# Kernel tuning notes

Measured on AMD Instinct MI355X. Metric: run time of the kernel, lower is better.

## Reference

```python
import jax, jax.numpy as jnp
import numpy as np


def setup_inputs() -> dict:
    key = jax.random.key(0)
    k1, k2, k3, k4, k5 = jax.random.split(key, 5)
    B, C, H, W = 8, 32, 64, 64
    inp = jax.random.normal(k1, (B, C, H, W), dtype=jnp.float32)
    # expected positions lie inside the image grid
    exPx = jax.random.uniform(k2, (B, H, W), dtype=jnp.float32) * (W - 1)
    exPy = jax.random.uniform(k3, (B, H, W), dtype=jnp.float32) * (H - 1)
    # positive Gaussian widths in roughly [1, 3]
    sigmax = jax.random.uniform(k4, (B, H, W), dtype=jnp.float32) * 2.0 + 1.0
    sigmay = jax.random.uniform(k5, (B, H, W), dtype=jnp.float32) * 2.0 + 1.0
    return {"input": inp, "exPx": exPx, "exPy": exPy,
            "sigmax": sigmax, "sigmay": sigmay}


def reference(input, exPx, exPy, sigmax, sigmay):
    """Gaussian-weighted spatial swap/warp (soft gather).

    For each output pixel (i, j):
      out[b,c,i,j] = sum_{u,v} G(u; exPy[b,i,j], sigmay[b,i,j])
                              * G(v; exPx[b,i,j], sigmax[b,i,j])
                              * input[b,c,u,v]  /  Z[b,i,j]
    where G is an unnormalized Gaussian and Z is the total weight mass.
    The 2D Gaussian weight is separable, so we contract rows then cols.
    """
    B, C, H, W = input.shape
    u = jnp.arange(H, dtype=input.dtype)  # source row coords (y)
    v = jnp.arange(W, dtype=input.dtype)  # source col coords (x)
    # wy: [B,H,W,H] weight over source rows u for each output pixel (i,j)
    wy = jnp.exp(-0.5 * ((u[None, None, None, :] - exPy[..., None]) / sigmay[..., None]) ** 2)
    # wx: [B,H,W,W] weight over source cols v
    wx = jnp.exp(-0.5 * ((v[None, None, None, :] - exPx[..., None]) / sigmax[..., None]) ** 2)
    # normalization mass per output pixel
    Z = wy.sum(-1) * wx.sum(-1) + jnp.asarray(1e-8, input.dtype)  # [B,H,W]
    # contract over source rows u -> [B,C,H,W,W]
    t = jnp.einsum('biju,bcuv->bcijv', wy, input)
    # contract over source cols v -> [B,C,H,W]
    out = jnp.einsum('bcijv,bijv->bcij', t, wx)
    return out / Z[:, None]
```

## Files before the change

### kernel.cpp

```cpp
#include <hip/hip_runtime.h>


#define BB 8
#define CC 32
#define HH 64
#define WW 64

typedef __attribute__((ext_vector_type(8))) short short8;
typedef __attribute__((ext_vector_type(4))) float f32x4;
typedef unsigned int uint;

__device__ __forceinline__ uint rn_bf16(float f) {
    uint u = __float_as_uint(f);
    return (u + 0x7FFFu + ((u >> 16) & 1u)) >> 16;
}

__global__ void preconvert_kernel(const float* __restrict__ x, uint* __restrict__ hi)
{
    const int n = BB * CC * HH * WW / 2;
    int idx = blockIdx.x * blockDim.x + threadIdx.x;
    for (; idx < n; idx += gridDim.x * blockDim.x) {
        const float2 d = ((const float2*)x)[idx];
        hi[idx] = rn_bf16(d.x) | (rn_bf16(d.y) << 16);
    }
}

#define WYS_OFF   0
#define WXH_OFF   16640
#define SUM_OFF   25856
#define INVZ_OFF  27904
#define LDS_BYTES 28160
#define RED_OFF   0

__global__ __launch_bounds__(256, 4)
void swap_mfma_kernel(const uint* __restrict__ xhi,
                      const float* __restrict__ exPx, const float* __restrict__ exPy,
                      const float* __restrict__ sigmax, const float* __restrict__ sigmay,
                      float* __restrict__ out)
{
    __shared__ __align__(16) char lds[LDS_BYTES];
    const int t    = threadIdx.x;
    const int lane = t & 63;
    const int w    = t >> 6;
    const int q    = (t >> 4) & 3;
    const int ln   = t & 15;
    const int bid   = blockIdx.x;
    const int b     = bid & 7;
    const int r     = bid >> 3;
    const int chalf = r & 1;
    const int i     = r >> 1;
    const int bi    = b * 64 + i;

    float* WYS = (float*)(lds + WYS_OFF);

    {
        const int p = lane;
        const int g = w;
        const int pixBase = bi * 64 + p;
        const float ey = exPy[pixBase], ex = exPx[pixBase];
        const float isy = 1.0f / sigmay[pixBase], isx = 1.0f / sigmax[pixBase];
        float sy = 0.0f, sx = 0.0f;
        #pragma unroll
        for (int k = 0; k < 16; ++k) {
            const int u = g * 16 + k;
            const float dy = ((float)u - ey) * isy;
            const float wy = __expf(-0.5f * dy * dy);
            WYS[u * 65 + p] = wy;
            sy += wy;
        }
        uint* WXH = (uint*)(lds + WXH_OFF);
        #pragma unroll
        for (int j = 0; j < 8; ++j) {
            const int v0 = g * 16 + 2 * j;
            const float dx0 = ((float)v0       - ex) * isx;
            const float dx1 = ((float)(v0 + 1) - ex) * isx;
            const float wx0 = __expf(-0.5f * dx0 * dx0);
            const float wx1 = __expf(-0.5f * dx1 * dx1);
            sx += wx0 + wx1;
            WXH[p * 36 + g * 8 + j] = rn_bf16(wx0) | (rn_bf16(wx1) << 16);
        }
        float* SUMY = (float*)(lds + SUM_OFF);
        float* SUMX = SUMY + 256;
        SUMY[g * 64 + p] = sy;
        SUMX[g * 64 + p] = sx;
    }
    __syncthreads();
    float* INVZ = (float*)(lds + INVZ_OFF);
    if (t < 64) {
        float* SUMY = (float*)(lds + SUM_OFF);
        float* SUMX = SUMY + 256;
        const float sy = SUMY[t] + SUMY[64 + t] + SUMY[128 + t] + SUMY[192 + t];
        const float sx = SUMX[t] + SUMX[64 + t] + SUMX[128 + t] + SUMX[192 + t];
        INVZ[t] = 1.0f / (sy * sx + 1e-8f);
    }
    __syncthreads();

    short8 bh[4][2];
    #pragma unroll
    for (int nt = 0; nt < 4; ++nt)
        #pragma unroll
        for (int ks = 0; ks < 2; ++ks)
            bh[nt][ks] = *(const short8*)(lds + WXH_OFF + (nt * 16 + ln) * 144 + ks * 64 + q * 16);
    float wyz[4][4];
    #pragma unroll
    for (int nt = 0; nt < 4; ++nt) {
        const float iz = INVZ[nt * 16 + ln];
        #pragma unroll
        for (int rr = 0; rr < 4; ++rr)
            wyz[nt][rr] = WYS[(w * 16 + q * 4 + rr) * 65 + nt * 16 + ln] * iz;
    }
    __syncthreads();

    const int cbase = b * CC + chalf * 16;
    float* RED = (float*)(lds + RED_OFF);
    const uint* xrow = xhi + (size_t)cbase * 2048 + (w * 16 + ln) * 32 + q * 4;

    #pragma unroll 4
    for (int c = 0; c < 16; ++c) {
        const uint4* src = (const uint4*)(xrow + (size_t)c * 2048);
        union { uint4 v; short8 s; } A0, A1;
        A0.v = src[0];
        A1.v = src[4];

        f32x4 acc[4];
        #pragma unroll
        for (int nt = 0; nt < 4; ++nt) acc[nt] = (f32x4){0.f, 0.f, 0.f, 0.f};
        #pragma unroll
        for (int nt = 0; nt < 4; ++nt) {
            acc[nt] = __builtin_amdgcn_mfma_f32_16x16x32_bf16(A0.s, bh[nt][0], acc[nt], 0, 0, 0);
            acc[nt] = __builtin_amdgcn_mfma_f32_16x16x32_bf16(A1.s, bh[nt][1], acc[nt], 0, 0, 0);
        }
        #pragma unroll
        for (int nt = 0; nt < 4; ++nt) {
            float ps = acc[nt][0] * wyz[nt][0] + acc[nt][1] * wyz[nt][1]
                     + acc[nt][2] * wyz[nt][2] + acc[nt][3] * wyz[nt][3];
            ps += __shfl_xor(ps, 16, 64);
            ps += __shfl_xor(ps, 32, 64);
            if (q == 0) RED[c * 256 + w * 64 + nt * 16 + ln] = ps;
        }
    }
    __syncthreads();

    {
        const int kk = t >> 6, p = t & 63;
        #pragma unroll
        for (int g = 0; g < 4; ++g) {
            const int c = g * 4 + kk;
            const float* Rk = RED + c * 256;
            const float o = Rk[p] + Rk[64 + p] + Rk[128 + p] + Rk[192 + p];
            out[(size_t)(cbase + c) * (HH * WW) + i * 64 + p] = o;
        }
    }
}

__device__ __forceinline__ void split_pair(float f0, float f1, uint& hi, uint& lo) {
    const uint u0 = __float_as_uint(f0), u1 = __float_as_uint(f1);
    hi = (u0 >> 16) | (u1 & 0xFFFF0000u);
    const float l0 = f0 - __uint_as_float(u0 & 0xFFFF0000u);
    const float l1 = f1 - __uint_as_float(u1 & 0xFFFF0000u);
    lo = (__float_as_uint(l0) >> 16) | (__float_as_uint(l1) & 0xFFFF0000u);
}

__global__ __launch_bounds__(256, 4)
void swap_fused_kernel(const float* __restrict__ inp,
                       const float* __restrict__ exPx, const float* __restrict__ exPy,
                       const float* __restrict__ sigmax, const float* __restrict__ sigmay,
                       float* __restrict__ out)
{
    __shared__ __align__(16) char lds[LDS_BYTES];
    const int t = threadIdx.x;
    const int lane = t & 63, w = t >> 6, q = (t >> 4) & 3, ln = t & 15;
    const int bid = blockIdx.x;
    const int b = bid & 7, r = bid >> 3;
    const int chalf = r & 1, i = r >> 1;
    const int bi = b * 64 + i;

    float* WYS = (float*)(lds + WYS_OFF);
    {
        const int p = lane, g = w;
        const int pixBase = bi * 64 + p;
        const float ey = exPy[pixBase], ex = exPx[pixBase];
        const float isy = 1.0f / sigmay[pixBase], isx = 1.0f / sigmax[pixBase];
        float sy = 0.0f, sx = 0.0f;
        #pragma unroll
        for (int k = 0; k < 16; ++k) {
            const int u = g * 16 + k;
            const float dy = ((float)u - ey) * isy;
            const float wy = __expf(-0.5f * dy * dy);
            WYS[u * 65 + p] = wy; sy += wy;
        }
        uint* WXH = (uint*)(lds + WXH_OFF);
        #pragma unroll
        for (int j = 0; j < 8; ++j) {
            const int v0 = g * 16 + 2 * j;
            const float dx0 = ((float)v0 - ex) * isx;
            const float dx1 = ((float)(v0 + 1) - ex) * isx;
            const float wx0 = __expf(-0.5f * dx0 * dx0);
            const float wx1 = __expf(-0.5f * dx1 * dx1);
            sx += wx0 + wx1;
            WXH[p * 36 + g * 8 + j] = rn_bf16(wx0) | (rn_bf16(wx1) << 16);
        }
        float* SUMY = (float*)(lds + SUM_OFF);
        float* SUMX = SUMY + 256;
        SUMY[g * 64 + p] = sy; SUMX[g * 64 + p] = sx;
    }
    __syncthreads();
    float* INVZ = (float*)(lds + INVZ_OFF);
    if (t < 64) {
        float* SUMY = (float*)(lds + SUM_OFF);
        float* SUMX = SUMY + 256;
        const float sy = SUMY[t] + SUMY[64 + t] + SUMY[128 + t] + SUMY[192 + t];
        const float sx = SUMX[t] + SUMX[64 + t] + SUMX[128 + t] + SUMX[192 + t];
        INVZ[t] = 1.0f / (sy * sx + 1e-8f);
    }
    __syncthreads();
    short8 bh[4][2];
    #pragma unroll
    for (int nt = 0; nt < 4; ++nt)
        #pragma unroll
        for (int ks = 0; ks < 2; ++ks)
            bh[nt][ks] = *(const short8*)(lds + WXH_OFF + (nt * 16 + ln) * 144 + ks * 64 + q * 16);
    float wyz[4][4];
    #pragma unroll
    for (int nt = 0; nt < 4; ++nt) {
        const float iz = INVZ[nt * 16 + ln];
        #pragma unroll
        for (int rr = 0; rr < 4; ++rr)
            wyz[nt][rr] = WYS[(w * 16 + q * 4 + rr) * 65 + nt * 16 + ln] * iz;
    }
    __syncthreads();
    const int cbase = b * CC + chalf * 16;
    float* RED = (float*)(lds + RED_OFF);
    const float* xrow = inp + (size_t)cbase * 4096 + (w * 16 + ln) * 64 + q * 8;
    #pragma unroll 2
    for (int c = 0; c < 16; ++c) {
        const float4* src = (const float4*)(xrow + (size_t)c * 4096);
        const float4 x0 = src[0], x1 = src[1], x2 = src[8], x3 = src[9];
        union { uint u[4]; short8 s; } Ah0, Al0, Ah1, Al1;
        split_pair(x0.x, x0.y, Ah0.u[0], Al0.u[0]);
        split_pair(x0.z, x0.w, Ah0.u[1], Al0.u[1]);
        split_pair(x1.x, x1.y, Ah0.u[2], Al0.u[2]);
        split_pair(x1.z, x1.w, Ah0.u[3], Al0.u[3]);
        split_pair(x2.x, x2.y, Ah1.u[0], Al1.u[0]);
        split_pair(x2.z, x2.w, Ah1.u[1], Al1.u[1]);
        split_pair(x3.x, x3.y, Ah1.u[2], Al1.u[2]);
        split_pair(x3.z, x3.w, Ah1.u[3], Al1.u[3]);
        f32x4 acc[4];
        #pragma unroll
        for (int nt = 0; nt < 4; ++nt) acc[nt] = (f32x4){0.f, 0.f, 0.f, 0.f};
        #pragma unroll
        for (int nt = 0; nt < 4; ++nt) {
            acc[nt] = __builtin_amdgcn_mfma_f32_16x16x32_bf16(Ah0.s, bh[nt][0], acc[nt], 0, 0, 0);
            acc[nt] = __builtin_amdgcn_mfma_f32_16x16x32_bf16(Al0.s, bh[nt][0], acc[nt], 0, 0, 0);
            acc[nt] = __builtin_amdgcn_mfma_f32_16x16x32_bf16(Ah1.s, bh[nt][1], acc[nt], 0, 0, 0);
            acc[nt] = __builtin_amdgcn_mfma_f32_16x16x32_bf16(Al1.s, bh[nt][1], acc[nt], 0, 0, 0);
        }
        #pragma unroll
        for (int nt = 0; nt < 4; ++nt) {
            float ps = acc[nt][0] * wyz[nt][0] + acc[nt][1] * wyz[nt][1]
                     + acc[nt][2] * wyz[nt][2] + acc[nt][3] * wyz[nt][3];
            ps += __shfl_xor(ps, 16, 64);
            ps += __shfl_xor(ps, 32, 64);
            if (q == 0) RED[c * 256 + w * 64 + nt * 16 + ln] = ps;
        }
    }
    __syncthreads();
    {
        const int kk = t >> 6, p = t & 63;
        #pragma unroll
        for (int g = 0; g < 4; ++g) {
            const int c = g * 4 + kk;
            const float* Rk = RED + c * 256;
            const float o = Rk[p] + Rk[64 + p] + Rk[128 + p] + Rk[192 + p];
            out[(size_t)(cbase + c) * (HH * WW) + i * 64 + p] = o;
        }
    }
}

extern "C" void kernel_launch(void* const* d_in, const int* in_sizes, int n_in,
                              void* d_out, int out_size, void* d_ws, size_t ws_size,
                              hipStream_t stream) {
    const float* inp    = (const float*)d_in[0];
    const float* exPx   = (const float*)d_in[1];
    const float* exPy   = (const float*)d_in[2];
    const float* sigmax = (const float*)d_in[3];
    const float* sigmay = (const float*)d_in[4];
    float* out = (float*)d_out;

    const size_t plane_bytes = (size_t)BB * CC * HH * WW * 2;
    if (ws_size >= plane_bytes) {
        uint* xhi = (uint*)d_ws;
        hipLaunchKernelGGL(preconvert_kernel, dim3(1024), dim3(256), 0, stream, inp, xhi);
        hipLaunchKernelGGL(swap_mfma_kernel, dim3(BB * HH * 2), dim3(256), 0, stream,
                           xhi, exPx, exPy, sigmax, sigmay, out);
    } else {
        hipLaunchKernelGGL(swap_fused_kernel, dim3(BB * HH * 2), dim3(256), 0, stream,
                           inp, exPx, exPy, sigmax, sigmay, out);
    }
}
```

Before: 82.25 us.

## Split channels across waves so each wave owns full rows, drop LDS reduction

The MFMA kernel now assigns four channels per wave, with each wave covering all 64 source rows through four M-tiles, instead of each wave covering 16 rows for all 16 channels. This removes the cross-wave LDS reduction buffer, the final syncthreads and the gather pass, and outputs are written directly after scaling by 1/Z. The Y-weights are stored transposed in LDS with float4 rows and read per tile inside the loop rather than cached in registers. The tradeoffs are more LDS reads in the inner loop, larger A-fragment register pressure, and a channel loop that is no longer unrolled.

Measured after the change: 97.01 us. 17.9% more time.

```diff
diff --git a/kernel.cpp b/kernel.cpp
--- a/kernel.cpp
+++ b/kernel.cpp
@@ -25,12 +25,11 @@
     }
 }
 
-#define WYS_OFF   0
-#define WXH_OFF   16640
-#define SUM_OFF   25856
-#define INVZ_OFF  27904
-#define LDS_BYTES 28160
-#define RED_OFF   0
+#define WYT_OFF   0
+#define WXH_OFF   17408
+#define SUM_OFF   26624
+#define INVZ_OFF  28672
+#define LDS_BYTES 28928
 
 __global__ __launch_bounds__(256, 4)
 void swap_mfma_kernel(const uint* __restrict__ xhi,
@@ -51,7 +50,7 @@
     const int i     = r >> 1;
     const int bi    = b * 64 + i;
 
-    float* WYS = (float*)(lds + WYS_OFF);
+    float* WYT = (float*)(lds + WYT_OFF);
 
     {
         const int p = lane;
@@ -61,12 +60,17 @@
         const float isy = 1.0f / sigmay[pixBase], isx = 1.0f / sigmax[pixBase];
         float sy = 0.0f, sx = 0.0f;
         #pragma unroll
-        for (int k = 0; k < 16; ++k) {
-            const int u = g * 16 + k;
-            const float dy = ((float)u - ey) * isy;
-            const float wy = __expf(-0.5f * dy * dy);
-            WYS[u * 65 + p] = wy;
-            sy += wy;
+        for (int jb = 0; jb < 4; ++jb) {
+            float4 wv;
+            #pragma unroll
+            for (int rr = 0; rr < 4; ++rr) {
+                const int u = g * 16 + jb * 4 + rr;
+                const float dy = ((float)u - ey) * isy;
+                const float wy = __expf(-0.5f * dy * dy);
+                ((float*)&wv)[rr] = wy;
+                sy += wy;
+            }
+            *(float4*)&WYT[p * 68 + g * 16 + jb * 4] = wv;
         }
         uint* WXH = (uint*)(lds + WXH_OFF);
         #pragma unroll
@@ -101,54 +105,37 @@
         #pragma unroll
         for (int ks = 0; ks < 2; ++ks)
             bh[nt][ks] = *(const short8*)(lds + WXH_OFF + (nt * 16 + ln) * 144 + ks * 64 + q * 16);
-    float wyz[4][4];
-    #pragma unroll
-    for (int nt = 0; nt < 4; ++nt) {
-        const float iz = INVZ[nt * 16 + ln];
-        #pragma unroll
-        for (int rr = 0; rr < 4; ++rr)
-            wyz[nt][rr] = WYS[(w * 16 + q * 4 + rr) * 65 + nt * 16 + ln] * iz;
-    }
-    __syncthreads();
-
-    const int cbase = b * CC + chalf * 16;
-    float* RED = (float*)(lds + RED_OFF);
-    const uint* xrow = xhi + (size_t)cbase * 2048 + (w * 16 + ln) * 32 + q * 4;
-
-    #pragma unroll 4
-    for (int c = 0; c < 16; ++c) {
-        const uint4* src = (const uint4*)(xrow + (size_t)c * 2048);
-        union { uint4 v; short8 s; } A0, A1;
-        A0.v = src[0];
-        A1.v = src[4];
-
-        f32x4 acc[4];
-        #pragma unroll
-        for (int nt = 0; nt < 4; ++nt) acc[nt] = (f32x4){0.f, 0.f, 0.f, 0.f};
+    float invz[4];
+    #pragma unroll
+    for (int nt = 0; nt < 4; ++nt) invz[nt] = INVZ[nt * 16 + ln];
+
+    const int cplane0 = b * CC + chalf * 16 + w * 4;
+    const uint* xbase = xhi + (size_t)cplane0 * 2048 + ln * 32 + q * 4;
+    float* obase = out + (size_t)cplane0 * 4096 + i * 64 + ln;
+
+    for (int c = 0; c < 4; ++c) {
+        const uint* xc = xbase + c * 2048;
+        union { uint4 v; short8 s; } A[4][2];
+        #pragma unroll
+        for (int mt = 0; mt < 4; ++mt) {
+            A[mt][0].v = *(const uint4*)(xc + mt * 512);
+            A[mt][1].v = *(const uint4*)(xc + mt * 512 + 16);
+        }
         #pragma unroll
         for (int nt = 0; nt < 4; ++nt) {
-            acc[nt] = __builtin_amdgcn_mfma_f32_16x16x32_bf16(A0.s, bh[nt][0], acc[nt], 0, 0, 0);
-            acc[nt] = __builtin_amdgcn_mfma_f32_16x16x32_bf16(A1.s, bh[nt][1], acc[nt], 0, 0, 0);
-        }
-        #pragma unroll
-        for (int nt = 0; nt < 4; ++nt) {
-            float ps = acc[nt][0] * wyz[nt][0] + acc[nt][1] * wyz[nt][1]
-                     + acc[nt][2] * wyz[nt][2] + acc[nt][3] * wyz[nt][3];
+            float ps = 0.0f;
+            #pragma unroll
+            for (int mt = 0; mt < 4; ++mt) {
+                f32x4 acc = (f32x4){0.f, 0.f, 0.f, 0.f};
+                acc = __builtin_amdgcn_mfma_f32_16x16x32_bf16(A[mt][0].s, bh[nt][0], acc, 0, 0, 0);
+                acc = __builtin_amdgcn_mfma_f32_16x16x32_bf16(A[mt][1].s, bh[nt][1], acc, 0, 0, 0);
+                const f32x4 wv = *(const f32x4*)&WYT[(nt * 16 + ln) * 68 + mt * 16 + q * 4];
+                ps += acc[0] * wv[0] + acc[1] * wv[1] + acc[2] * wv[2] + acc[3] * wv[3];
+            }
             ps += __shfl_xor(ps, 16, 64);
             ps += __shfl_xor(ps, 32, 64);
-            if (q == 0) RED[c * 256 + w * 64 + nt * 16 + ln] = ps;
-        }
-    }
-    __syncthreads();
-
-    {
-        const int kk = t >> 6, p = t & 63;
-        #pragma unroll
-        for (int g = 0; g < 4; ++g) {
-            const int c = g * 4 + kk;
-            const float* Rk = RED + c * 256;
-            const float o = Rk[p] + Rk[64 + p] + Rk[128 + p] + Rk[192 + p];
-            out[(size_t)(cbase + c) * (HH * WW) + i * 64 + p] = o;
+            if (q == 0)
+                obase[(size_t)c * 4096 + nt * 16] = ps * invz[nt];
         }
     }
 }
@@ -161,13 +148,20 @@
     lo = (__float_as_uint(l0) >> 16) | (__float_as_uint(l1) & 0xFFFF0000u);
 }
 
+#define FB_WYS_OFF   0
+#define FB_WXH_OFF   16640
+#define FB_SUM_OFF   25856
+#define FB_INVZ_OFF  27904
+#define FB_LDS_BYTES 28160
+#define FB_RED_OFF   0
+
 __global__ __launch_bounds__(256, 4)
 void swap_fused_kernel(const float* __restrict__ inp,
                        const float* __restrict__ exPx, const float* __restrict__ exPy,
                        const float* __restrict__ sigmax, const float* __restrict__ sigmay,
                        float* __restrict__ out)
 {
-    __shared__ __align__(16) char lds[LDS_BYTES];
+    __shared__ __align__(16) char lds[FB_LDS_BYTES];
     const int t = threadIdx.x;
     const int lane = t & 63, w = t >> 6, q = (t >> 4) & 3, ln = t & 15;
     const int bid = blockIdx.x;
@@ -175,7 +169,7 @@
     const int chalf = r & 1, i = r >> 1;
     const int bi = b * 64 + i;
 
-    float* WYS = (float*)(lds + WYS_OFF);
+    float* WYS = (float*)(lds + FB_WYS_OFF);
     {
         const int p = lane, g = w;
         const int pixBase = bi * 64 + p;
@@ -189,7 +183,7 @@
             const float wy = __expf(-0.5f * dy * dy);
             WYS[u * 65 + p] = wy; sy += wy;
         }
-        uint* WXH = (uint*)(lds + WXH_OFF);
+        uint* WXH = (uint*)(lds + FB_WXH_OFF);
         #pragma unroll
         for (int j = 0; j < 8; ++j) {
             const int v0 = g * 16 + 2 * j;
@@ -200,14 +194,14 @@
             sx += wx0 + wx1;
             WXH[p * 36 + g * 8 + j] = rn_bf16(wx0) | (rn_bf16(wx1) << 16);
         }
-        float* SUMY = (float*)(lds + SUM_OFF);
+        float* SUMY = (float*)(lds + FB_SUM_OFF);
         float* SUMX = SUMY + 256;
         SUMY[g * 64 + p] = sy; SUMX[g * 64 + p] = sx;
     }
     __syncthreads();
-    float* INVZ = (float*)(lds + INVZ_OFF);
+    float* INVZ = (float*)(lds + FB_INVZ_OFF);
     if (t < 64) {
-        float* SUMY = (float*)(lds + SUM_OFF);
+        float* SUMY = (float*)(lds + FB_SUM_OFF);
         float* SUMX = SUMY + 256;
         const float sy = SUMY[t] + SUMY[64 + t] + SUMY[128 + t] + SUMY[192 + t];
         const float sx = SUMX[t] + SUMX[64 + t] + SUMX[128 + t] + SUMX[192 + t];
@@ -219,7 +213,7 @@
     for (int nt = 0; nt < 4; ++nt)
         #pragma unroll
         for (int ks = 0; ks < 2; ++ks)
-            bh[nt][ks] = *(const short8*)(lds + WXH_OFF + (nt * 16 + ln) * 144 + ks * 64 + q * 16);
+            bh[nt][ks] = *(const short8*)(lds + FB_WXH_OFF + (nt * 16 + ln) * 144 + ks * 64 + q * 16);
     float wyz[4][4];
     #pragma unroll
     for (int nt = 0; nt < 4; ++nt) {
@@ -230,7 +224,7 @@
     }
     __syncthreads();
     const int cbase = b * CC + chalf * 16;
-    float* RED = (float*)(lds + RED_OFF);
+    float* RED = (float*)(lds + FB_RED_OFF);
     const float* xrow = inp + (size_t)cbase * 4096 + (w * 16 + ln) * 64 + q * 8;
     #pragma unroll 2
     for (int c = 0; c < 16; ++c) {
```
